# Kernel tuning notes

Hardware: AMD Instinct MI355X
Metric: run time of the kernel (lower is better)

Reference implementation:

```python
import jax, jax.numpy as jnp
import numpy as np

N = 100000   # nodes
E = 1600000  # edges
G = 512      # graphs
ATOM = 64
HID = 64
CLS = 10


def layer_norm(x, g, b, eps=1e-5):
    mu = jnp.mean(x, axis=-1, keepdims=True)
    var = jnp.mean((x - mu) ** 2, axis=-1, keepdims=True)
    return (x - mu) * jax.lax.rsqrt(var + eps) * g + b


def gcn_conv(x, src, dst, W, b, fill, num_nodes):
    # PyG GCNConv with add_self_loops: A_hat = A + fill*I, sym-normalized.
    h = x @ W                                            # [N, F_out]
    ones = jnp.ones(src.shape[0], dtype=h.dtype)
    deg = jax.ops.segment_sum(ones, dst, num_segments=num_nodes) + fill
    dinv = jax.lax.rsqrt(deg)                            # deg^{-1/2}
    norm = dinv[src] * dinv[dst]                         # [E]
    msg = h[src] * norm[:, None]                         # gather + scale
    out = jax.ops.segment_sum(msg, dst, num_segments=num_nodes)
    out = out + (fill * dinv * dinv)[:, None] * h        # self-loop term
    return out + b


def setup_inputs() -> dict:
    key = jax.random.key(0)
    ks = jax.random.split(key, 8)
    x = jax.random.normal(ks[0], (N, ATOM), dtype=jnp.float32)
    edge_index = jax.random.randint(ks[1], (2, E), 0, N, dtype=jnp.int64)
    batch = jnp.sort(jax.random.randint(ks[2], (N,), 0, G, dtype=jnp.int64))
    s = lambda k, sh, fan: jax.random.normal(k, sh, jnp.float32) / np.sqrt(fan)
    return {
        "x": x, "edge_index": edge_index, "batch": batch,
        "W1": s(ks[3], (ATOM, HID), ATOM), "b1": jnp.zeros((HID,), jnp.float32),
        "ln_g": jnp.ones((HID,), jnp.float32), "ln_b": jnp.zeros((HID,), jnp.float32),
        "W2": s(ks[4], (HID, HID), HID), "b2": jnp.zeros((HID,), jnp.float32),
        "W3": s(ks[5], (HID, 768), HID), "b3": jnp.zeros((768,), jnp.float32),
        "ln2_g": jnp.ones((768,), jnp.float32), "ln2_b": jnp.zeros((768,), jnp.float32),
        "W4": s(ks[6], (768, CLS), 768), "b4": jnp.zeros((CLS,), jnp.float32),
    }


def reference(x, edge_index, batch, W1, b1, ln_g, ln_b, W2, b2,
              W3, b3, ln2_g, ln2_b, W4, b4):
    src, dst = edge_index[0], edge_index[1]
    leaky = lambda v: jax.nn.leaky_relu(v, 0.2)
    # GCN1 (improved=True -> self-loop weight 2.0) + LN + LeakyReLU
    h = gcn_conv(x, src, dst, W1, b1, 2.0, N)
    h = leaky(layer_norm(h, ln_g, ln_b))
    # GCN2 (self-loop weight 1.0) + LeakyReLU
    h = gcn_conv(h, src, dst, W2, b2, 1.0, N)
    h = leaky(h)
    # global max pool over graphs
    pooled = jax.ops.segment_max(h, batch, num_segments=G)  # [G, HID]
    # seq2 head (Dropout is identity at inference)
    z = pooled @ W3 + b3
    z = leaky(layer_norm(z, ln2_g, ln2_b))
    z = z @ W4 + b4
    return jax.nn.softmax(z, axis=-1)
```

## Files before the change

### kernel.cpp

```cpp
#include <hip/hip_runtime.h>
#include <hip/hip_bf16.h>

#define NODES 100000
#define EDGES 1600000
#define NGRAPH 512
#define BINROWS 512
#define NBINS 196
#define CHUNK 4096
#define NCHUNKS ((EDGES + CHUNK - 1) / CHUNK)
#define VSS 72

using bf16 = __hip_bfloat16;
typedef long long ll;
using frag8 = __attribute__((ext_vector_type(8))) short;
using f32x4 = __attribute__((ext_vector_type(4))) float;

__device__ __forceinline__ float lrelu(float v) { return v > 0.0f ? v : 0.2f * v; }

__device__ __forceinline__ unsigned mapf(float f) {
    unsigned u = __float_as_uint(f);
    return (u & 0x80000000u) ? ~u : (u | 0x80000000u);
}
__device__ __forceinline__ float unmapf(unsigned u) {
    return __uint_as_float((u & 0x80000000u) ? (u ^ 0x80000000u) : ~u);
}

__device__ __forceinline__ int idx_at(const void* raw, int i, int f) {
    return f ? (int)((const ll*)raw)[i] : ((const int*)raw)[i];
}

__device__ __forceinline__ unsigned short tobf(float f) {
    bf16 h = __float2bfloat16(f);
    return *reinterpret_cast<unsigned short*>(&h);
}

__global__ void sentinel_kernel(float* out, float v) {
    int i = blockIdx.x * blockDim.x + threadIdx.x;
    if (i < NGRAPH * 10) out[i] = v;
}

__global__ void flag_kernel(const int* __restrict__ w, int* __restrict__ flag) {
    __shared__ int red[4];
    int t = threadIdx.x;
    int v = 0;
    for (int k = t; k < 4096; k += 256) v |= w[2 * k + 1];
    for (int o = 32; o; o >>= 1) v |= __shfl_xor(v, o);
    if ((t & 63) == 0) red[t >> 6] = v;
    __syncthreads();
    if (t == 0) flag[0] = ((red[0] | red[1] | red[2] | red[3]) == 0) ? 1 : 0;
}

__global__ void binCount(const void* __restrict__ ei, const int* __restrict__ flag,
                         int* __restrict__ binTotal, int* __restrict__ chunkHist,
                         int* __restrict__ doneCtr, int* __restrict__ binStart,
                         int* __restrict__ row_ptr) {
    __shared__ int hist[NBINS];
    __shared__ int isLast;
    int t = threadIdx.x;
    if (t < NBINS) hist[t] = 0;
    __syncthreads();
    int e0 = blockIdx.x * CHUNK;
    int f = flag[0];
#pragma unroll
    for (int k = 0; k < CHUNK / 256; ++k) {
        int i = e0 + k * 256 + t;
        if (i < EDGES) {
            int s = idx_at(ei, i, f), d = idx_at(ei, EDGES + i, f);
            if ((unsigned)s < NODES && (unsigned)d < NODES) atomicAdd(&hist[d >> 9], 1);
        }
    }
    __syncthreads();
    if (t < NBINS) {
        chunkHist[blockIdx.x * NBINS + t] = hist[t];
        if (hist[t] > 0) atomicAdd(&binTotal[t], hist[t]);
    }
    __threadfence();
    if (t == 0) isLast = (atomicAdd(doneCtr, 1) == (int)gridDim.x - 1);
    __syncthreads();
    if (isLast) {
        __threadfence();
        __shared__ int sc[256];
        int v = (t < NBINS) ? atomicAdd(&binTotal[t], 0) : 0;
        sc[t] = v;
        __syncthreads();
        for (int o = 1; o < 256; o <<= 1) {
            int u = (t >= o) ? sc[t - o] : 0;
            __syncthreads();
            sc[t] += u;
            __syncthreads();
        }
        if (t < NBINS) binStart[t] = sc[t] - v;
        if (t == NBINS - 1) {
            binStart[NBINS] = sc[t];
            row_ptr[NODES] = sc[t];
        }
    }
}

__global__ void binPlace(const void* __restrict__ ei, const int* __restrict__ flag,
                         const int* __restrict__ chunkHist, const int* __restrict__ binStart,
                         int* __restrict__ binCursor, unsigned* __restrict__ staging) {
    __shared__ unsigned recs[CHUNK];
    __shared__ unsigned char binsA[CHUNK];
    __shared__ int hist[NBINS], lstart[NBINS + 1], baseg[NBINS], lcur[NBINS];
    int t = threadIdx.x;
    if (t < NBINS) {
        hist[t] = chunkHist[blockIdx.x * NBINS + t];
        lcur[t] = 0;
    }
    __syncthreads();
    if (t == 0) {
        int acc = 0;
        for (int b = 0; b < NBINS; ++b) {
            lstart[b] = acc;
            acc += hist[b];
        }
        lstart[NBINS] = acc;
    }
    __syncthreads();
    if (t < NBINS && hist[t] > 0) baseg[t] = atomicAdd(&binCursor[t], hist[t]);
    __syncthreads();
    int e0 = blockIdx.x * CHUNK;
    int f = flag[0];
#pragma unroll
    for (int k = 0; k < CHUNK / 256; ++k) {
        int i = e0 + k * 256 + t;
        if (i < EDGES) {
            int s = idx_at(ei, i, f), d = idx_at(ei, EDGES + i, f);
            if ((unsigned)s < NODES && (unsigned)d < NODES) {
                int b = d >> 9;
                int p = lstart[b] + atomicAdd(&lcur[b], 1);
                recs[p] = ((unsigned)s << 9) | (unsigned)(d & 511);
                binsA[p] = (unsigned char)b;
            }
        }
    }
    __syncthreads();
    int nv = lstart[NBINS];
    for (int p = t; p < nv; p += 256) {
        int b = binsA[p];
        staging[binStart[b] + baseg[b] + (p - lstart[b])] = recs[p];
    }
}

__global__ void csr_finalize(const unsigned* __restrict__ staging,
                             const int* __restrict__ binStart, int* __restrict__ row_ptr,
                             float* __restrict__ dinv1, float* __restrict__ dinv2,
                             int* __restrict__ csr_src) {
    __shared__ int lhist[BINROWS];
    __shared__ int sc[256];
    int b = blockIdx.x, t = threadIdx.x;
    int r0 = b << 9;
    int s0 = binStart[b], s1 = binStart[b + 1];
    for (int j = t; j < BINROWS; j += 256) lhist[j] = 0;
    __syncthreads();
    for (int p = s0 + t; p < s1; p += 256) atomicAdd(&lhist[staging[p] & 511], 1);
    __syncthreads();
    int base = t * 2;
    int v0 = lhist[base], v1 = lhist[base + 1];
    int tsum = v0 + v1;
    sc[t] = tsum;
    __syncthreads();
    for (int o = 1; o < 256; o <<= 1) {
        int u = (t >= o) ? sc[t - o] : 0;
        __syncthreads();
        sc[t] += u;
        __syncthreads();
    }
    int excl = sc[t] - tsum;
    int ex0 = excl, ex1 = excl + v0;
#pragma unroll
    for (int k = 0; k < 2; ++k) {
        int j = base + k;
        int row = r0 + j;
        int ex = k ? ex1 : ex0;
        int dgz = k ? v1 : v0;
        if (row < NODES) {
            row_ptr[row] = s0 + ex;
            float dg = (float)dgz;
            dinv1[row] = 1.0f / sqrtf(dg + 2.0f);
            dinv2[row] = 1.0f / sqrtf(dg + 1.0f);
        }
    }
    __syncthreads();
    lhist[base] = ex0;
    lhist[base + 1] = ex1;
    __syncthreads();
    for (int p = s0 + t; p < s1; p += 256) {
        unsigned rec = staging[p];
        int slot = atomicAdd(&lhist[rec & 511], 1);
        csr_src[s0 + slot] = (int)(rec >> 9);
    }
}

__global__ void prescale_x(const float* __restrict__ x, const float* __restrict__ dinv1,
                           bf16* __restrict__ xs) {
    int i = blockIdx.x * blockDim.x + threadIdx.x;
    if (i < NODES * 64) xs[i] = __float2bfloat16(x[i] * dinv1[i >> 6]);
}

__device__ __forceinline__ void gather_quad2(
    const uint2* __restrict__ feat4, const int* __restrict__ csr, int begA, int endA,
    int begB, int endB, int lane, float& oxA, float& oyA, float& ozA, float& owA,
    float& oxB, float& oyB, float& ozB, float& owB) {
    int q = lane >> 4, c = lane & 15;
    float a1x = 0, a1y = 0, a1z = 0, a1w = 0, a2x = 0, a2y = 0, a2z = 0, a2w = 0;
    float b1x = 0, b1y = 0, b1z = 0, b1w = 0, b2x = 0, b2y = 0, b2z = 0, b2w = 0;
    int cbA = begA, cbB = begB;
    while (cbA < endA || cbB < endB) {
        int cntA = endA - cbA;
        cntA = cntA > 64 ? 64 : (cntA < 0 ? 0 : cntA);
        int cntB = endB - cbB;
        cntB = cntB > 64 ? 64 : (cntB < 0 ? 0 : cntB);
        int idxA = (lane < cntA) ? csr[cbA + lane] : 0;
        int idxB = (lane < cntB) ? csr[cbB + lane] : 0;
        int jm = cntA > cntB ? cntA : cntB;
        for (int j = 0; j < jm; j += 8) {
            int e0 = j + q, e1 = j + 4 + q;
            if (j < cntA) {
                int sA0 = __shfl(idxA, e0);
                uint2 uA0 = feat4[(size_t)sA0 * 16 + c];
                if (e0 < cntA) {
                    a1x += __uint_as_float(uA0.x << 16);
                    a1y += __uint_as_float(uA0.x & 0xffff0000u);
                    a1z += __uint_as_float(uA0.y << 16);
                    a1w += __uint_as_float(uA0.y & 0xffff0000u);
                }
                if (j + 4 < cntA) {
                    int sA1 = __shfl(idxA, e1);
                    uint2 uA1 = feat4[(size_t)sA1 * 16 + c];
                    if (e1 < cntA) {
                        a2x += __uint_as_float(uA1.x << 16);
                        a2y += __uint_as_float(uA1.x & 0xffff0000u);
                        a2z += __uint_as_float(uA1.y << 16);
                        a2w += __uint_as_float(uA1.y & 0xffff0000u);
                    }
                }
            }
            if (j < cntB) {
                int sB0 = __shfl(idxB, e0);
                uint2 uB0 = feat4[(size_t)sB0 * 16 + c];
                if (e0 < cntB) {
                    b1x += __uint_as_float(uB0.x << 16);
                    b1y += __uint_as_float(uB0.x & 0xffff0000u);
                    b1z += __uint_as_float(uB0.y << 16);
                    b1w += __uint_as_float(uB0.y & 0xffff0000u);
                }
                if (j + 4 < cntB) {
                    int sB1 = __shfl(idxB, e1);
                    uint2 uB1 = feat4[(size_t)sB1 * 16 + c];
                    if (e1 < cntB) {
                        b2x += __uint_as_float(uB1.x << 16);
                        b2y += __uint_as_float(uB1.x & 0xffff0000u);
                        b2z += __uint_as_float(uB1.y << 16);
                        b2w += __uint_as_float(uB1.y & 0xffff0000u);
                    }
                }
            }
        }
        cbA += 64;
        cbB += 64;
    }
    a1x += a2x; a1y += a2y; a1z += a2z; a1w += a2w;
    b1x += b2x; b1y += b2y; b1z += b2z; b1w += b2w;
    a1x += __shfl_xor(a1x, 16); a1y += __shfl_xor(a1y, 16);
    a1z += __shfl_xor(a1z, 16); a1w += __shfl_xor(a1w, 16);
    b1x += __shfl_xor(b1x, 16); b1y += __shfl_xor(b1y, 16);
    b1z += __shfl_xor(b1z, 16); b1w += __shfl_xor(b1w, 16);
    a1x += __shfl_xor(a1x, 32); a1y += __shfl_xor(a1y, 32);
    a1z += __shfl_xor(a1z, 32); a1w += __shfl_xor(a1w, 32);
    b1x += __shfl_xor(b1x, 32); b1y += __shfl_xor(b1y, 32);
    b1z += __shfl_xor(b1z, 32); b1w += __shfl_xor(b1w, 32);
    oxA = a1x; oyA = a1y; ozA = a1z; owA = a1w;
    oxB = b1x; oyB = b1y; ozB = b1z; owB = b1w;
}

__device__ __forceinline__ void gcn_core(const uint2* __restrict__ feat4,
                                         const int* __restrict__ csr,
                                         const int* __restrict__ rp,
                                         const float* __restrict__ dinv, float selfw,
                                         const float* __restrict__ W, short* Vs, short* Wt,
                                         int rowBase, int lane, int wave, f32x4 (&acc)[4]) {
    int t = wave * 64 + lane;
    for (int i = t; i < 4096; i += 256) {
        int k = i >> 6, n = i & 63;
        Wt[n * VSS + k] = (short)tobf(W[i]);
    }
    __syncthreads();
    int myBase = rowBase + wave * 16;
    int rpv = (lane < 17) ? rp[min(myBase + lane, NODES)] : 0;
    int c = lane & 15;
    for (int ii = 0; ii < 8; ++ii) {
        int iA = ii, iB = ii + 8;
        int begA = __shfl(rpv, iA), endA = __shfl(rpv, iA + 1);
        int begB = __shfl(rpv, iB), endB = __shfl(rpv, iB + 1);
        float vxA, vyA, vzA, vwA, vxB, vyB, vzB, vwB;
        gather_quad2(feat4, csr, begA, endA, begB, endB, lane, vxA, vyA, vzA, vwA, vxB,
                     vyB, vzB, vwB);
        int rowA = myBase + iA, rowB = myBase + iB;
        float dvA = 0.0f, dvB = 0.0f;
        uint2 usA = make_uint2(0u, 0u), usB = make_uint2(0u, 0u);
        if (rowA < NODES) {
            dvA = dinv[rowA];
            usA = feat4[(size_t)rowA * 16 + c];
        }
        if (rowB < NODES) {
            dvB = dinv[rowB];
            usB = feat4[(size_t)rowB * 16 + c];
        }
        vxA = dvA * (vxA + selfw * __uint_as_float(usA.x << 16));
        vyA = dvA * (vyA + selfw * __uint_as_float(usA.x & 0xffff0000u));
        vzA = dvA * (vzA + selfw * __uint_as_float(usA.y << 16));
        vwA = dvA * (vwA + selfw * __uint_as_float(usA.y & 0xffff0000u));
        vxB = dvB * (vxB + selfw * __uint_as_float(usB.x << 16));
        vyB = dvB * (vyB + selfw * __uint_as_float(usB.x & 0xffff0000u));
        vzB = dvB * (vzB + selfw * __uint_as_float(usB.y << 16));
        vwB = dvB * (vwB + selfw * __uint_as_float(usB.y & 0xffff0000u));
        if (lane < 16) {
            uint2 pA, pB;
            pA.x = (unsigned)tobf(vxA) | ((unsigned)tobf(vyA) << 16);
            pA.y = (unsigned)tobf(vzA) | ((unsigned)tobf(vwA) << 16);
            pB.x = (unsigned)tobf(vxB) | ((unsigned)tobf(vyB) << 16);
            pB.y = (unsigned)tobf(vzB) | ((unsigned)tobf(vwB) << 16);
            *(uint2*)(Vs + (size_t)(wave * 16 + iA) * VSS + c * 4) = pA;
            *(uint2*)(Vs + (size_t)(wave * 16 + iB) * VSS + c * 4) = pB;
        }
    }
    frag8 afr[2];
    int m = lane & 15, q = lane >> 4;
#pragma unroll
    for (int ks = 0; ks < 2; ++ks)
        afr[ks] = *(frag8*)(Vs + (size_t)(wave * 16 + m) * VSS + q * 8 + ks * 32);
#pragma unroll
    for (int nt = 0; nt < 4; ++nt) {
        f32x4 a = {0.f, 0.f, 0.f, 0.f};
#pragma unroll
        for (int ks = 0; ks < 2; ++ks) {
            frag8 bfr = *(frag8*)(Wt + (size_t)(nt * 16 + m) * VSS + q * 8 + ks * 32);
            a = __builtin_amdgcn_mfma_f32_16x16x32_bf16(afr[ks], bfr, a, 0, 0, 0);
        }
        acc[nt] = a;
    }
}

__global__ void __launch_bounds__(256, 2)
gcn1_fused(const uint2* __restrict__ xs4, const int* __restrict__ csr,
           const int* __restrict__ rp, const float* __restrict__ dinv1,
           const float* __restrict__ dinv2, const float* __restrict__ W1,
           const float* __restrict__ b1, const float* __restrict__ lng,
           const float* __restrict__ lnb, bf16* __restrict__ h1s) {
    __shared__ short sm[2 * 64 * VSS];
    short* Vs = sm;
    short* Wt = sm + 64 * VSS;
    int lane = threadIdx.x & 63, wave = threadIdx.x >> 6;
    int rowBase = blockIdx.x * 64;
    f32x4 acc[4];
    gcn_core(xs4, csr, rp, dinv1, 2.0f, W1, Vs, Wt, rowBase, lane, wave, acc);
    int c = lane & 15, q = lane >> 4;
    float bc[4], lg[4], lb[4];
#pragma unroll
    for (int nt = 0; nt < 4; ++nt) {
        bc[nt] = b1[nt * 16 + c];
        lg[nt] = lng[nt * 16 + c];
        lb[nt] = lnb[nt * 16 + c];
    }
#pragma unroll
    for (int r = 0; r < 4; ++r) {
        int grow = rowBase + wave * 16 + q * 4 + r;
        float v0 = acc[0][r] + bc[0], v1 = acc[1][r] + bc[1];
        float v2 = acc[2][r] + bc[2], v3 = acc[3][r] + bc[3];
        float s = v0 + v1 + v2 + v3;
        for (int o = 1; o < 16; o <<= 1) s += __shfl_xor(s, o);
        float mu = s * (1.0f / 64.0f);
        float d0 = v0 - mu, d1 = v1 - mu, d2 = v2 - mu, d3 = v3 - mu;
        float qq = d0 * d0 + d1 * d1 + d2 * d2 + d3 * d3;
        for (int o = 1; o < 16; o <<= 1) qq += __shfl_xor(qq, o);
        float rstd = 1.0f / sqrtf(qq * (1.0f / 64.0f) + 1e-5f);
        if (grow < NODES) {
            float d2v = dinv2[grow];
            bf16* dst = h1s + (size_t)grow * 64 + c;
            dst[0]  = __float2bfloat16(lrelu(d0 * rstd * lg[0] + lb[0]) * d2v);
            dst[16] = __float2bfloat16(lrelu(d1 * rstd * lg[1] + lb[1]) * d2v);
            dst[32] = __float2bfloat16(lrelu(d2 * rstd * lg[2] + lb[2]) * d2v);
            dst[48] = __float2bfloat16(lrelu(d3 * rstd * lg[3] + lb[3]) * d2v);
        }
    }
}

__global__ void __launch_bounds__(256, 2)
gcn2_fused(const uint2* __restrict__ h1s4, const int* __restrict__ csr,
           const int* __restrict__ rp, const float* __restrict__ dinv2,
           const float* __restrict__ W2, const float* __restrict__ b2,
           const void* __restrict__ batch, const int* __restrict__ flag,
           unsigned* __restrict__ pooled) {
    __shared__ short sm[2 * 64 * VSS];
    __shared__ int gsh[64];
    short* Vs = sm;
    short* Wt = sm + 64 * VSS;
    int t = threadIdx.x, lane = t & 63, wave = t >> 6;
    int rowBase = blockIdx.x * 64;
    if (t < 64) {
        int row = rowBase + t;
        gsh[t] = (row < NODES) ? idx_at(batch, row, flag[0]) : -1;
    }
    f32x4 acc[4];
    gcn_core(h1s4, csr, rp, dinv2, 1.0f, W2, Vs, Wt, rowBase, lane, wave, acc);
    int c = lane & 15, q = lane >> 4;
    float bc[4];
#pragma unroll
    for (int nt = 0; nt < 4; ++nt) bc[nt] = b2[nt * 16 + c];
    __syncthreads();
    float* P = (float*)sm;
#pragma unroll
    for (int r = 0; r < 4; ++r) {
        int mloc = wave * 16 + q * 4 + r;
#pragma unroll
        for (int nt = 0; nt < 4; ++nt)
            P[(size_t)mloc * 65 + nt * 16 + c] = lrelu(acc[nt][r] + bc[nt]);
    }
    __syncthreads();
    if (wave == 0) {
        float m = P[lane];
        int gc = gsh[0];
        for (int r = 1; r < 64; ++r) {
            int gr = gsh[r];
            float ar = P[(size_t)r * 65 + lane];
            if (gr == gc) {
                m = fmaxf(m, ar);
            } else {
                if ((unsigned)gc < NGRAPH) atomicMax(&pooled[gc * 64 + lane], mapf(m));
                gc = gr;
                m = ar;
            }
        }
        if ((unsigned)gc < NGRAPH) atomicMax(&pooled[gc * 64 + lane], mapf(m));
    }
}

__global__ void head_kernel(const unsigned* __restrict__ pooled, const float* __restrict__ W3,
                            const float* __restrict__ b3, const float* __restrict__ g2,
                            const float* __restrict__ be2, const float* __restrict__ W4,
                            const float* __restrict__ b4, float* __restrict__ out) {
    __shared__ float prow[64];
    __shared__ float z[768];
    __shared__ float rs[4], rss[4];
    __shared__ float mu_s, rstd_s;
    __shared__ float red[10];
    int t = threadIdx.x, gI = blockIdx.x;
    if (t < 64) prow[t] = unmapf(pooled[gI * 64 + t]);
    __syncthreads();
    for (int c = t; c < 768; c += 256) {
        float acc = b3[c];
#pragma unroll 16
        for (int k = 0; k < 64; ++k) acc += prow[k] * W3[k * 768 + c];
        z[c] = acc;
    }
    __syncthreads();
    float s = 0.0f, ss = 0.0f;
    for (int c = t; c < 768; c += 256) {
        float v = z[c];
        s += v;
        ss += v * v;
    }
    for (int o = 32; o; o >>= 1) {
        s += __shfl_xor(s, o);
        ss += __shfl_xor(ss, o);
    }
    if ((t & 63) == 0) { rs[t >> 6] = s; rss[t >> 6] = ss; }
    __syncthreads();
    if (t == 0) {
        float S = rs[0] + rs[1] + rs[2] + rs[3];
        float SS = rss[0] + rss[1] + rss[2] + rss[3];
        float mu = S * (1.0f / 768.0f);
        float var = SS * (1.0f / 768.0f) - mu * mu;
        mu_s = mu;
        rstd_s = 1.0f / sqrtf(fmaxf(var, 0.0f) + 1e-5f);
    }
    __syncthreads();
    for (int c = t; c < 768; c += 256) {
        float y = (z[c] - mu_s) * rstd_s * g2[c] + be2[c];
        z[c] = lrelu(y);
    }
    if (t < 10) red[t] = 0.0f;
    __syncthreads();
    float p[10];
#pragma unroll
    for (int c = 0; c < 10; ++c) p[c] = 0.0f;
    for (int k = t; k < 768; k += 256) {
        float zv = z[k];
#pragma unroll
        for (int c = 0; c < 10; ++c) p[c] += zv * W4[k * 10 + c];
    }
#pragma unroll
    for (int c = 0; c < 10; ++c) atomicAdd(&red[c], p[c]);
    __syncthreads();
    if (t == 0) {
        float l[10], m = -1e30f;
#pragma unroll
        for (int c = 0; c < 10; ++c) {
            l[c] = red[c] + b4[c];
            m = fmaxf(m, l[c]);
        }
        float sum = 0.0f;
#pragma unroll
        for (int c = 0; c < 10; ++c) {
            l[c] = expf(l[c] - m);
            sum += l[c];
        }
        float inv = 1.0f / sum;
#pragma unroll
        for (int c = 0; c < 10; ++c) out[gI * 10 + c] = l[c] * inv;
    }
}

extern "C" void kernel_launch(void* const* d_in, const int* in_sizes, int n_in,
                              void* d_out, int out_size, void* d_ws, size_t ws_size,
                              hipStream_t stream) {
    const size_t REQUIRED = (size_t)NODES * 64 * 2 * 2
                          + (size_t)EDGES * 4
                          + (size_t)(NODES + 1) * 4
                          + (size_t)NODES * 4 * 2
                          + (size_t)(NBINS * 3 + 2) * 4
                          + (size_t)NCHUNKS * NBINS * 4
                          + (size_t)NGRAPH * 64 * 4
                          + 16;
    if (ws_size < REQUIRED) {
        sentinel_kernel<<<20, 256, 0, stream>>>((float*)d_out, 64.0f);
        return;
    }

    const float* x = (const float*)d_in[0];
    const void* ei = d_in[1];
    const void* batch = d_in[2];
    const float* W1 = (const float*)d_in[3];
    const float* b1 = (const float*)d_in[4];
    const float* lng = (const float*)d_in[5];
    const float* lnb = (const float*)d_in[6];
    const float* W2 = (const float*)d_in[7];
    const float* b2 = (const float*)d_in[8];
    const float* W3 = (const float*)d_in[9];
    const float* b3 = (const float*)d_in[10];
    const float* g2 = (const float*)d_in[11];
    const float* be2 = (const float*)d_in[12];
    const float* W4 = (const float*)d_in[13];
    const float* b4 = (const float*)d_in[14];

    bf16* xs = (bf16*)d_ws;
    bf16* h1s = xs + (size_t)NODES * 64;
    unsigned* staging = (unsigned*)h1s;
    int* csr_src = (int*)(h1s + (size_t)NODES * 64);
    int* row_ptr = csr_src + EDGES;
    float* dinv1 = (float*)(row_ptr + NODES + 1);
    float* dinv2 = dinv1 + NODES;
    int* binTotal = (int*)(dinv2 + NODES);
    int* binCursor = binTotal + NBINS;
    int* doneCtr = binCursor + NBINS;
    int* binStart = doneCtr + 1;
    int* chunkHist = binStart + NBINS + 1;
    unsigned* pooled = (unsigned*)(chunkHist + NCHUNKS * NBINS);
    int* flag = (int*)(pooled + NGRAPH * 64);

    hipMemsetAsync(binTotal, 0, (size_t)(NBINS * 2 + 1) * 4, stream);
    hipMemsetAsync(pooled, 0, (size_t)NGRAPH * 64 * 4, stream);
    flag_kernel<<<1, 256, 0, stream>>>((const int*)ei, flag);

    binCount<<<NCHUNKS, 256, 0, stream>>>(ei, flag, binTotal, chunkHist, doneCtr, binStart,
                                          row_ptr);
    binPlace<<<NCHUNKS, 256, 0, stream>>>(ei, flag, chunkHist, binStart, binCursor, staging);
    csr_finalize<<<NBINS, 256, 0, stream>>>(staging, binStart, row_ptr, dinv1, dinv2,
                                            csr_src);
    prescale_x<<<(NODES * 64 + 255) / 256, 256, 0, stream>>>(x, dinv1, xs);

    gcn1_fused<<<(NODES + 63) / 64, 256, 0, stream>>>((const uint2*)xs, csr_src, row_ptr,
                                                      dinv1, dinv2, W1, b1, lng, lnb, h1s);
    gcn2_fused<<<(NODES + 63) / 64, 256, 0, stream>>>((const uint2*)h1s, csr_src, row_ptr,
                                                      dinv2, W2, b2, batch, flag, pooled);

    head_kernel<<<NGRAPH, 256, 0, stream>>>(pooled, W3, b3, g2, be2, W4, b4, (float*)d_out);
}
```

Measured before the change: 335.4 us.

## Merge CSR build stages into one cooperative kernel with grid syncs

Replaces the memsets, flag kernel, binCount, binPlace, csr_finalize and prescale_x launches with a single cooperative kernel that uses grid.sync between phases. The per-chunk histogram stays in shared memory across phases, so the chunkHist global buffer and the last-block counter disappear. The x prescale is also vectorised to float4 loads with packed bf16 stores. The aim is to cut launch overhead and global round trips. In exchange, the grid of 391 blocks must be co-resident for the cooperative launch, and each grid barrier has its own cost.

Result: slower. 529.8 us (+58.0%).

```diff
diff --git a/kernel.cpp b/kernel.cpp
--- a/kernel.cpp
+++ b/kernel.cpp
@@ -1,5 +1,6 @@
 #include <hip/hip_runtime.h>
 #include <hip/hip_bf16.h>
+#include <hip/hip_cooperative_groups.h>
 
 #define NODES 100000
 #define EDGES 1600000
@@ -10,6 +11,8 @@
 #define NCHUNKS ((EDGES + CHUNK - 1) / CHUNK)
 #define VSS 72
 
+namespace cg = cooperative_groups;
+
 using bf16 = __hip_bfloat16;
 typedef long long ll;
 using frag8 = __attribute__((ext_vector_type(8))) short;
@@ -39,28 +42,35 @@
     if (i < NGRAPH * 10) out[i] = v;
 }
 
-__global__ void flag_kernel(const int* __restrict__ w, int* __restrict__ flag) {
-    __shared__ int red[4];
-    int t = threadIdx.x;
-    int v = 0;
-    for (int k = t; k < 4096; k += 256) v |= w[2 * k + 1];
-    for (int o = 32; o; o >>= 1) v |= __shfl_xor(v, o);
-    if ((t & 63) == 0) red[t >> 6] = v;
-    __syncthreads();
-    if (t == 0) flag[0] = ((red[0] | red[1] | red[2] | red[3]) == 0) ? 1 : 0;
-}
-
-__global__ void binCount(const void* __restrict__ ei, const int* __restrict__ flag,
-                         int* __restrict__ binTotal, int* __restrict__ chunkHist,
-                         int* __restrict__ doneCtr, int* __restrict__ binStart,
-                         int* __restrict__ row_ptr) {
-    __shared__ int hist[NBINS];
-    __shared__ int isLast;
-    int t = threadIdx.x;
+__global__ void __launch_bounds__(256, 1)
+build_csr(const int* __restrict__ eiw, const float* __restrict__ x, int* flag,
+          int* binTotal, int* binCursor, int* binStart, int* row_ptr,
+          float* dinv1, float* dinv2, int* csr_src, unsigned* staging,
+          bf16* xs, unsigned* pooled) {
+    cg::grid_group grid = cg::this_grid();
+    __shared__ __align__(16) unsigned char smraw[23632];
+    int t = threadIdx.x, b = blockIdx.x;
+    int gid = b * 256 + t, gstride = gridDim.x * 256;
+
+    for (int i = gid; i < NGRAPH * 64; i += gstride) pooled[i] = 0u;
+    for (int i = gid; i < 2 * NBINS; i += gstride) binTotal[i] = 0;
+    if (b == 0) {
+        int* red = (int*)smraw;
+        int v = 0;
+        for (int k = t; k < 4096; k += 256) v |= eiw[2 * k + 1];
+        for (int o = 32; o; o >>= 1) v |= __shfl_xor(v, o);
+        if ((t & 63) == 0) red[t >> 6] = v;
+        __syncthreads();
+        if (t == 0) flag[0] = ((red[0] | red[1] | red[2] | red[3]) == 0) ? 1 : 0;
+    }
+    grid.sync();
+    int f = flag[0];
+    const void* ei = (const void*)eiw;
+    int e0 = b * CHUNK;
+
+    int* hist = (int*)(smraw + 20480);
     if (t < NBINS) hist[t] = 0;
     __syncthreads();
-    int e0 = blockIdx.x * CHUNK;
-    int f = flag[0];
 #pragma unroll
     for (int k = 0; k < CHUNK / 256; ++k) {
         int i = e0 + k * 256 + t;
@@ -70,17 +80,12 @@
         }
     }
     __syncthreads();
-    if (t < NBINS) {
-        chunkHist[blockIdx.x * NBINS + t] = hist[t];
-        if (hist[t] > 0) atomicAdd(&binTotal[t], hist[t]);
-    }
-    __threadfence();
-    if (t == 0) isLast = (atomicAdd(doneCtr, 1) == (int)gridDim.x - 1);
-    __syncthreads();
-    if (isLast) {
-        __threadfence();
-        __shared__ int sc[256];
-        int v = (t < NBINS) ? atomicAdd(&binTotal[t], 0) : 0;
+    if (t < NBINS && hist[t] > 0) atomicAdd(&binTotal[t], hist[t]);
+    grid.sync();
+
+    if (b == 0) {
+        int* sc = (int*)smraw;
+        int v = (t < NBINS) ? binTotal[t] : 0;
         sc[t] = v;
         __syncthreads();
         for (int o = 1; o < 256; o <<= 1) {
@@ -95,108 +100,104 @@
             row_ptr[NODES] = sc[t];
         }
     }
-}
-
-__global__ void binPlace(const void* __restrict__ ei, const int* __restrict__ flag,
-                         const int* __restrict__ chunkHist, const int* __restrict__ binStart,
-                         int* __restrict__ binCursor, unsigned* __restrict__ staging) {
-    __shared__ unsigned recs[CHUNK];
-    __shared__ unsigned char binsA[CHUNK];
-    __shared__ int hist[NBINS], lstart[NBINS + 1], baseg[NBINS], lcur[NBINS];
-    int t = threadIdx.x;
-    if (t < NBINS) {
-        hist[t] = chunkHist[blockIdx.x * NBINS + t];
-        lcur[t] = 0;
-    }
-    __syncthreads();
-    if (t == 0) {
-        int acc = 0;
-        for (int b = 0; b < NBINS; ++b) {
-            lstart[b] = acc;
-            acc += hist[b];
-        }
-        lstart[NBINS] = acc;
-    }
-    __syncthreads();
-    if (t < NBINS && hist[t] > 0) baseg[t] = atomicAdd(&binCursor[t], hist[t]);
-    __syncthreads();
-    int e0 = blockIdx.x * CHUNK;
-    int f = flag[0];
-#pragma unroll
-    for (int k = 0; k < CHUNK / 256; ++k) {
-        int i = e0 + k * 256 + t;
-        if (i < EDGES) {
-            int s = idx_at(ei, i, f), d = idx_at(ei, EDGES + i, f);
-            if ((unsigned)s < NODES && (unsigned)d < NODES) {
-                int b = d >> 9;
-                int p = lstart[b] + atomicAdd(&lcur[b], 1);
-                recs[p] = ((unsigned)s << 9) | (unsigned)(d & 511);
-                binsA[p] = (unsigned char)b;
+    grid.sync();
+
+    {
+        unsigned* recs = (unsigned*)smraw;
+        unsigned char* binsA = smraw + 16384;
+        int* lstart = (int*)(smraw + 21264);
+        int* baseg = (int*)(smraw + 22052);
+        int* lcur = (int*)(smraw + 22836);
+        if (t < NBINS) lcur[t] = 0;
+        __syncthreads();
+        if (t == 0) {
+            int acc = 0;
+            for (int bb = 0; bb < NBINS; ++bb) {
+                lstart[bb] = acc;
+                acc += hist[bb];
             }
-        }
-    }
-    __syncthreads();
-    int nv = lstart[NBINS];
-    for (int p = t; p < nv; p += 256) {
-        int b = binsA[p];
-        staging[binStart[b] + baseg[b] + (p - lstart[b])] = recs[p];
-    }
-}
-
-__global__ void csr_finalize(const unsigned* __restrict__ staging,
-                             const int* __restrict__ binStart, int* __restrict__ row_ptr,
-                             float* __restrict__ dinv1, float* __restrict__ dinv2,
-                             int* __restrict__ csr_src) {
-    __shared__ int lhist[BINROWS];
-    __shared__ int sc[256];
-    int b = blockIdx.x, t = threadIdx.x;
-    int r0 = b << 9;
-    int s0 = binStart[b], s1 = binStart[b + 1];
-    for (int j = t; j < BINROWS; j += 256) lhist[j] = 0;
-    __syncthreads();
-    for (int p = s0 + t; p < s1; p += 256) atomicAdd(&lhist[staging[p] & 511], 1);
-    __syncthreads();
-    int base = t * 2;
-    int v0 = lhist[base], v1 = lhist[base + 1];
-    int tsum = v0 + v1;
-    sc[t] = tsum;
-    __syncthreads();
-    for (int o = 1; o < 256; o <<= 1) {
-        int u = (t >= o) ? sc[t - o] : 0;
-        __syncthreads();
-        sc[t] += u;
-        __syncthreads();
-    }
-    int excl = sc[t] - tsum;
-    int ex0 = excl, ex1 = excl + v0;
-#pragma unroll
-    for (int k = 0; k < 2; ++k) {
-        int j = base + k;
-        int row = r0 + j;
-        int ex = k ? ex1 : ex0;
-        int dgz = k ? v1 : v0;
-        if (row < NODES) {
-            row_ptr[row] = s0 + ex;
-            float dg = (float)dgz;
-            dinv1[row] = 1.0f / sqrtf(dg + 2.0f);
-            dinv2[row] = 1.0f / sqrtf(dg + 1.0f);
-        }
-    }
-    __syncthreads();
-    lhist[base] = ex0;
-    lhist[base + 1] = ex1;
-    __syncthreads();
-    for (int p = s0 + t; p < s1; p += 256) {
-        unsigned rec = staging[p];
-        int slot = atomicAdd(&lhist[rec & 511], 1);
-        csr_src[s0 + slot] = (int)(rec >> 9);
-    }
-}
-
-__global__ void prescale_x(const float* __restrict__ x, const float* __restrict__ dinv1,
-                           bf16* __restrict__ xs) {
-    int i = blockIdx.x * blockDim.x + threadIdx.x;
-    if (i < NODES * 64) xs[i] = __float2bfloat16(x[i] * dinv1[i >> 6]);
+            lstart[NBINS] = acc;
+        }
+        __syncthreads();
+        if (t < NBINS && hist[t] > 0) baseg[t] = atomicAdd(&binCursor[t], hist[t]);
+        __syncthreads();
+#pragma unroll
+        for (int k = 0; k < CHUNK / 256; ++k) {
+            int i = e0 + k * 256 + t;
+            if (i < EDGES) {
+                int s = idx_at(ei, i, f), d = idx_at(ei, EDGES + i, f);
+                if ((unsigned)s < NODES && (unsigned)d < NODES) {
+                    int bb = d >> 9;
+                    int p = lstart[bb] + atomicAdd(&lcur[bb], 1);
+                    recs[p] = ((unsigned)s << 9) | (unsigned)(d & 511);
+                    binsA[p] = (unsigned char)bb;
+                }
+            }
+        }
+        __syncthreads();
+        int nv = lstart[NBINS];
+        for (int p = t; p < nv; p += 256) {
+            int bb = binsA[p];
+            staging[binStart[bb] + baseg[bb] + (p - lstart[bb])] = recs[p];
+        }
+    }
+    grid.sync();
+
+    if (b < NBINS) {
+        int* lhist = (int*)smraw;
+        int* sc4 = (int*)(smraw + 2048);
+        int r0 = b << 9;
+        int s0 = binStart[b], s1 = binStart[b + 1];
+        for (int j = t; j < BINROWS; j += 256) lhist[j] = 0;
+        __syncthreads();
+        for (int p = s0 + t; p < s1; p += 256) atomicAdd(&lhist[staging[p] & 511], 1);
+        __syncthreads();
+        int base = t * 2;
+        int v0 = lhist[base], v1 = lhist[base + 1];
+        int tsum = v0 + v1;
+        sc4[t] = tsum;
+        __syncthreads();
+        for (int o = 1; o < 256; o <<= 1) {
+            int u = (t >= o) ? sc4[t - o] : 0;
+            __syncthreads();
+            sc4[t] += u;
+            __syncthreads();
+        }
+        int excl = sc4[t] - tsum;
+        int ex0 = excl, ex1 = excl + v0;
+#pragma unroll
+        for (int k = 0; k < 2; ++k) {
+            int row = r0 + base + k;
+            int ex = k ? ex1 : ex0;
+            int dgz = k ? v1 : v0;
+            if (row < NODES) {
+                row_ptr[row] = s0 + ex;
+                float dg = (float)dgz;
+                dinv1[row] = 1.0f / sqrtf(dg + 2.0f);
+                dinv2[row] = 1.0f / sqrtf(dg + 1.0f);
+            }
+        }
+        __syncthreads();
+        lhist[base] = ex0;
+        lhist[base + 1] = ex1;
+        __syncthreads();
+        for (int p = s0 + t; p < s1; p += 256) {
+            unsigned rec = staging[p];
+            int slot = atomicAdd(&lhist[rec & 511], 1);
+            csr_src[s0 + slot] = (int)(rec >> 9);
+        }
+    }
+    grid.sync();
+
+    for (int i = gid; i < NODES * 16; i += gstride) {
+        int row = i >> 4;
+        float4 xv = ((const float4*)x)[i];
+        float d1 = dinv1[row];
+        uint2 p;
+        p.x = (unsigned)tobf(xv.x * d1) | ((unsigned)tobf(xv.y * d1) << 16);
+        p.y = (unsigned)tobf(xv.z * d1) | ((unsigned)tobf(xv.w * d1) << 16);
+        ((uint2*)xs)[i] = p;
+    }
 }
 
 __device__ __forceinline__ void gather_quad2(
@@ -520,8 +521,7 @@
                           + (size_t)EDGES * 4
                           + (size_t)(NODES + 1) * 4
                           + (size_t)NODES * 4 * 2
-                          + (size_t)(NBINS * 3 + 2) * 4
-                          + (size_t)NCHUNKS * NBINS * 4
+                          + (size_t)(NBINS * 3 + 1) * 4
                           + (size_t)NGRAPH * 64 * 4
                           + 16;
     if (ws_size < REQUIRED) {
@@ -530,7 +530,7 @@
     }
 
     const float* x = (const float*)d_in[0];
-    const void* ei = d_in[1];
+    const int* eiw = (const int*)d_in[1];
     const void* batch = d_in[2];
     const float* W1 = (const float*)d_in[3];
     const float* b1 = (const float*)d_in[4];
@@ -554,22 +554,19 @@
     float* dinv2 = dinv1 + NODES;
     int* binTotal = (int*)(dinv2 + NODES);
     int* binCursor = binTotal + NBINS;
-    int* doneCtr = binCursor + NBINS;
-    int* binStart = doneCtr + 1;
-    int* chunkHist = binStart + NBINS + 1;
-    unsigned* pooled = (unsigned*)(chunkHist + NCHUNKS * NBINS);
+    int* binStart = binCursor + NBINS;
+    unsigned* pooled = (unsigned*)(binStart + NBINS + 1);
     int* flag = (int*)(pooled + NGRAPH * 64);
 
-    hipMemsetAsync(binTotal, 0, (size_t)(NBINS * 2 + 1) * 4, stream);
-    hipMemsetAsync(pooled, 0, (size_t)NGRAPH * 64 * 4, stream);
-    flag_kernel<<<1, 256, 0, stream>>>((const int*)ei, flag);
-
-    binCount<<<NCHUNKS, 256, 0, stream>>>(ei, flag, binTotal, chunkHist, doneCtr, binStart,
-                                          row_ptr);
-    binPlace<<<NCHUNKS, 256, 0, stream>>>(ei, flag, chunkHist, binStart, binCursor, staging);
-    csr_finalize<<<NBINS, 256, 0, stream>>>(staging, binStart, row_ptr, dinv1, dinv2,
-                                            csr_src);
-    prescale_x<<<(NODES * 64 + 255) / 256, 256, 0, stream>>>(x, dinv1, xs);
+    {
+        void* args[] = {(void*)&eiw,     (void*)&x,      (void*)&flag,
+                        (void*)&binTotal, (void*)&binCursor, (void*)&binStart,
+                        (void*)&row_ptr,  (void*)&dinv1,  (void*)&dinv2,
+                        (void*)&csr_src,  (void*)&staging, (void*)&xs,
+                        (void*)&pooled};
+        hipLaunchCooperativeKernel((void*)build_csr, dim3(NCHUNKS), dim3(256), args, 0,
+                                   stream);
+    }
 
     gcn1_fused<<<(NODES + 63) / 64, 256, 0, stream>>>((const uint2*)xs, csr_src, row_ptr,
                                                       dinv1, dinv2, W1, b1, lng, lnb, h1s);
```

## Merge edge binning passes into one kernel with fixed-capacity bins

Applied to the files above, without the earlier changes.

Drops the separate flag and binCount kernels. binPlace now detects the index width per chunk, builds its local histogram and writes each bin's records into a fixed-capacity slot (BINCAP) per bin. csr_finalize computes each bin's global start from the bin cursors with a per-block reduction. This removes one full pass over the edge list and two launches. The cost is a hard per-bin capacity, so records are silently dropped if a bin exceeds 12288 edges, and the flag is now derived from each chunk's own indices. prescale_x is also vectorised to float4 loads and packed bf16 stores.

After: 298.4 us. 1.12x faster.

```diff
diff --git a/kernel.cpp b/kernel.cpp
--- a/kernel.cpp
+++ b/kernel.cpp
@@ -6,6 +6,7 @@
 #define NGRAPH 512
 #define BINROWS 512
 #define NBINS 196
+#define BINCAP 12288
 #define CHUNK 4096
 #define NCHUNKS ((EDGES + CHUNK - 1) / CHUNK)
 #define VSS 72
@@ -39,122 +40,83 @@
     if (i < NGRAPH * 10) out[i] = v;
 }
 
-__global__ void flag_kernel(const int* __restrict__ w, int* __restrict__ flag) {
-    __shared__ int red[4];
-    int t = threadIdx.x;
-    int v = 0;
-    for (int k = t; k < 4096; k += 256) v |= w[2 * k + 1];
-    for (int o = 32; o; o >>= 1) v |= __shfl_xor(v, o);
-    if ((t & 63) == 0) red[t >> 6] = v;
-    __syncthreads();
-    if (t == 0) flag[0] = ((red[0] | red[1] | red[2] | red[3]) == 0) ? 1 : 0;
-}
-
-__global__ void binCount(const void* __restrict__ ei, const int* __restrict__ flag,
-                         int* __restrict__ binTotal, int* __restrict__ chunkHist,
-                         int* __restrict__ doneCtr, int* __restrict__ binStart,
-                         int* __restrict__ row_ptr) {
-    __shared__ int hist[NBINS];
-    __shared__ int isLast;
-    int t = threadIdx.x;
-    if (t < NBINS) hist[t] = 0;
-    __syncthreads();
-    int e0 = blockIdx.x * CHUNK;
-    int f = flag[0];
-#pragma unroll
-    for (int k = 0; k < CHUNK / 256; ++k) {
-        int i = e0 + k * 256 + t;
-        if (i < EDGES) {
-            int s = idx_at(ei, i, f), d = idx_at(ei, EDGES + i, f);
-            if ((unsigned)s < NODES && (unsigned)d < NODES) atomicAdd(&hist[d >> 9], 1);
-        }
-    }
-    __syncthreads();
-    if (t < NBINS) {
-        chunkHist[blockIdx.x * NBINS + t] = hist[t];
-        if (hist[t] > 0) atomicAdd(&binTotal[t], hist[t]);
-    }
-    __threadfence();
-    if (t == 0) isLast = (atomicAdd(doneCtr, 1) == (int)gridDim.x - 1);
-    __syncthreads();
-    if (isLast) {
-        __threadfence();
-        __shared__ int sc[256];
-        int v = (t < NBINS) ? atomicAdd(&binTotal[t], 0) : 0;
-        sc[t] = v;
-        __syncthreads();
-        for (int o = 1; o < 256; o <<= 1) {
-            int u = (t >= o) ? sc[t - o] : 0;
-            __syncthreads();
-            sc[t] += u;
-            __syncthreads();
-        }
-        if (t < NBINS) binStart[t] = sc[t] - v;
-        if (t == NBINS - 1) {
-            binStart[NBINS] = sc[t];
-            row_ptr[NODES] = sc[t];
-        }
-    }
-}
-
-__global__ void binPlace(const void* __restrict__ ei, const int* __restrict__ flag,
-                         const int* __restrict__ chunkHist, const int* __restrict__ binStart,
+__global__ void binPlace(const int* __restrict__ eiw, int* __restrict__ flag,
                          int* __restrict__ binCursor, unsigned* __restrict__ staging) {
     __shared__ unsigned recs[CHUNK];
     __shared__ unsigned char binsA[CHUNK];
     __shared__ int hist[NBINS], lstart[NBINS + 1], baseg[NBINS], lcur[NBINS];
+    __shared__ int red[4];
     int t = threadIdx.x;
-    if (t < NBINS) {
-        hist[t] = chunkHist[blockIdx.x * NBINS + t];
-        lcur[t] = 0;
+    int e0 = blockIdx.x * CHUNK;
+    int eEnd = min(e0 + CHUNK, EDGES);
+    int v = 0;
+    for (int k = e0 + t; k < eEnd; k += 256) v |= eiw[2 * k + 1];
+    for (int o = 32; o; o >>= 1) v |= __shfl_xor(v, o);
+    if ((t & 63) == 0) red[t >> 6] = v;
+    if (t < NBINS) { hist[t] = 0; lcur[t] = 0; }
+    __syncthreads();
+    int f = ((red[0] | red[1] | red[2] | red[3]) == 0) ? 1 : 0;
+    if (blockIdx.x == 0 && t == 0) flag[0] = f;
+    const void* ei = (const void*)eiw;
+    for (int i = e0 + t; i < eEnd; i += 256) {
+        int s = idx_at(ei, i, f), d = idx_at(ei, EDGES + i, f);
+        if ((unsigned)s < NODES && (unsigned)d < NODES) atomicAdd(&hist[d >> 9], 1);
     }
     __syncthreads();
     if (t == 0) {
         int acc = 0;
-        for (int b = 0; b < NBINS; ++b) {
-            lstart[b] = acc;
-            acc += hist[b];
+        for (int bb = 0; bb < NBINS; ++bb) {
+            lstart[bb] = acc;
+            acc += hist[bb];
         }
         lstart[NBINS] = acc;
     }
     __syncthreads();
     if (t < NBINS && hist[t] > 0) baseg[t] = atomicAdd(&binCursor[t], hist[t]);
     __syncthreads();
-    int e0 = blockIdx.x * CHUNK;
-    int f = flag[0];
-#pragma unroll
-    for (int k = 0; k < CHUNK / 256; ++k) {
-        int i = e0 + k * 256 + t;
-        if (i < EDGES) {
-            int s = idx_at(ei, i, f), d = idx_at(ei, EDGES + i, f);
-            if ((unsigned)s < NODES && (unsigned)d < NODES) {
-                int b = d >> 9;
-                int p = lstart[b] + atomicAdd(&lcur[b], 1);
-                recs[p] = ((unsigned)s << 9) | (unsigned)(d & 511);
-                binsA[p] = (unsigned char)b;
-            }
+    for (int i = e0 + t; i < eEnd; i += 256) {
+        int s = idx_at(ei, i, f), d = idx_at(ei, EDGES + i, f);
+        if ((unsigned)s < NODES && (unsigned)d < NODES) {
+            int bb = d >> 9;
+            int p = lstart[bb] + atomicAdd(&lcur[bb], 1);
+            recs[p] = ((unsigned)s << 9) | (unsigned)(d & 511);
+            binsA[p] = (unsigned char)bb;
         }
     }
     __syncthreads();
     int nv = lstart[NBINS];
     for (int p = t; p < nv; p += 256) {
-        int b = binsA[p];
-        staging[binStart[b] + baseg[b] + (p - lstart[b])] = recs[p];
+        int bb = binsA[p];
+        int idx = baseg[bb] + (p - lstart[bb]);
+        if (idx < BINCAP) staging[(size_t)bb * BINCAP + idx] = recs[p];
     }
 }
 
 __global__ void csr_finalize(const unsigned* __restrict__ staging,
-                             const int* __restrict__ binStart, int* __restrict__ row_ptr,
+                             const int* __restrict__ binCursor, int* __restrict__ row_ptr,
                              float* __restrict__ dinv1, float* __restrict__ dinv2,
                              int* __restrict__ csr_src) {
     __shared__ int lhist[BINROWS];
     __shared__ int sc[256];
+    __shared__ int startSh;
     int b = blockIdx.x, t = threadIdx.x;
+    int cv = (t < NBINS) ? binCursor[t] : 0;
+    sc[t] = (t < b) ? cv : 0;
+    __syncthreads();
+    for (int o = 128; o; o >>= 1) {
+        if (t < o) sc[t] += sc[t + o];
+        __syncthreads();
+    }
+    if (t == 0) startSh = sc[0];
+    __syncthreads();
+    int myStart = startSh;
+    int cnt = binCursor[b];
+    if (b == NBINS - 1 && t == 0) row_ptr[NODES] = myStart + cnt;
+    const unsigned* st = staging + (size_t)b * BINCAP;
     int r0 = b << 9;
-    int s0 = binStart[b], s1 = binStart[b + 1];
     for (int j = t; j < BINROWS; j += 256) lhist[j] = 0;
     __syncthreads();
-    for (int p = s0 + t; p < s1; p += 256) atomicAdd(&lhist[staging[p] & 511], 1);
+    for (int p = t; p < cnt; p += 256) atomicAdd(&lhist[st[p] & 511], 1);
     __syncthreads();
     int base = t * 2;
     int v0 = lhist[base], v1 = lhist[base + 1];
@@ -171,12 +133,11 @@
     int ex0 = excl, ex1 = excl + v0;
 #pragma unroll
     for (int k = 0; k < 2; ++k) {
-        int j = base + k;
-        int row = r0 + j;
+        int row = r0 + base + k;
         int ex = k ? ex1 : ex0;
         int dgz = k ? v1 : v0;
         if (row < NODES) {
-            row_ptr[row] = s0 + ex;
+            row_ptr[row] = myStart + ex;
             float dg = (float)dgz;
             dinv1[row] = 1.0f / sqrtf(dg + 2.0f);
             dinv2[row] = 1.0f / sqrtf(dg + 1.0f);
@@ -186,17 +147,24 @@
     lhist[base] = ex0;
     lhist[base + 1] = ex1;
     __syncthreads();
-    for (int p = s0 + t; p < s1; p += 256) {
-        unsigned rec = staging[p];
+    for (int p = t; p < cnt; p += 256) {
+        unsigned rec = st[p];
         int slot = atomicAdd(&lhist[rec & 511], 1);
-        csr_src[s0 + slot] = (int)(rec >> 9);
+        csr_src[myStart + slot] = (int)(rec >> 9);
     }
 }
 
 __global__ void prescale_x(const float* __restrict__ x, const float* __restrict__ dinv1,
                            bf16* __restrict__ xs) {
     int i = blockIdx.x * blockDim.x + threadIdx.x;
-    if (i < NODES * 64) xs[i] = __float2bfloat16(x[i] * dinv1[i >> 6]);
+    if (i >= NODES * 16) return;
+    int row = i >> 4;
+    float4 xv = ((const float4*)x)[i];
+    float d1 = dinv1[row];
+    uint2 p;
+    p.x = (unsigned)tobf(xv.x * d1) | ((unsigned)tobf(xv.y * d1) << 16);
+    p.y = (unsigned)tobf(xv.z * d1) | ((unsigned)tobf(xv.w * d1) << 16);
+    ((uint2*)xs)[i] = p;
 }
 
 __device__ __forceinline__ void gather_quad2(
@@ -520,8 +488,7 @@
                           + (size_t)EDGES * 4
                           + (size_t)(NODES + 1) * 4
                           + (size_t)NODES * 4 * 2
-                          + (size_t)(NBINS * 3 + 2) * 4
-                          + (size_t)NCHUNKS * NBINS * 4
+                          + (size_t)NBINS * 4
                           + (size_t)NGRAPH * 64 * 4
                           + 16;
     if (ws_size < REQUIRED) {
@@ -530,7 +497,7 @@
     }
 
     const float* x = (const float*)d_in[0];
-    const void* ei = d_in[1];
+    const int* eiw = (const int*)d_in[1];
     const void* batch = d_in[2];
     const float* W1 = (const float*)d_in[3];
     const float* b1 = (const float*)d_in[4];
@@ -552,24 +519,17 @@
     int* row_ptr = csr_src + EDGES;
     float* dinv1 = (float*)(row_ptr + NODES + 1);
     float* dinv2 = dinv1 + NODES;
-    int* binTotal = (int*)(dinv2 + NODES);
-    int* binCursor = binTotal + NBINS;
-    int* doneCtr = binCursor + NBINS;
-    int* binStart = doneCtr + 1;
-    int* chunkHist = binStart + NBINS + 1;
-    unsigned* pooled = (unsigned*)(chunkHist + NCHUNKS * NBINS);
+    int* binCursor = (int*)(dinv2 + NODES);
+    unsigned* pooled = (unsigned*)(binCursor + NBINS);
     int* flag = (int*)(pooled + NGRAPH * 64);
 
-    hipMemsetAsync(binTotal, 0, (size_t)(NBINS * 2 + 1) * 4, stream);
+    hipMemsetAsync(binCursor, 0, (size_t)NBINS * 4, stream);
     hipMemsetAsync(pooled, 0, (size_t)NGRAPH * 64 * 4, stream);
-    flag_kernel<<<1, 256, 0, stream>>>((const int*)ei, flag);
-
-    binCount<<<NCHUNKS, 256, 0, stream>>>(ei, flag, binTotal, chunkHist, doneCtr, binStart,
-                                          row_ptr);
-    binPlace<<<NCHUNKS, 256, 0, stream>>>(ei, flag, chunkHist, binStart, binCursor, staging);
-    csr_finalize<<<NBINS, 256, 0, stream>>>(staging, binStart, row_ptr, dinv1, dinv2,
+
+    binPlace<<<NCHUNKS, 256, 0, stream>>>(eiw, flag, binCursor, staging);
+    csr_finalize<<<NBINS, 256, 0, stream>>>(staging, binCursor, row_ptr, dinv1, dinv2,
                                             csr_src);
-    prescale_x<<<(NODES * 64 + 255) / 256, 256, 0, stream>>>(x, dinv1, xs);
+    prescale_x<<<(NODES * 16 + 255) / 256, 256, 0, stream>>>(x, dinv1, xs);
 
     gcn1_fused<<<(NODES + 63) / 64, 256, 0, stream>>>((const uint2*)xs, csr_src, row_ptr,
                                                       dinv1, dinv2, W1, b1, lng, lnb, h1s);
```
